# Optimization experiments

Measured on AMD Instinct MI355X. Metric: run time of the kernel, lower is better.

The kernel has to match this reference:

```python
import jax, jax.numpy as jnp
import numpy as np

N_NODES = 20000
N_EDGES = 320000
IN_DIM = 128
HID = 256
HEADS = 8
DH = HID // HEADS  # 32
LAYERS = 3
NUM_GRAPHS = 64
OUT_DIM = 10
SLOPE = 0.2  # DGL GATv2Conv default negative_slope


def setup_inputs() -> dict:
    key = jax.random.key(0)
    ks = jax.random.split(key, 20)
    s_in = 1.0 / np.sqrt(IN_DIM)
    s_h = 1.0 / np.sqrt(HID)
    s_h2 = 1.0 / np.sqrt(HID // 2)
    return {
        "feature": jax.random.normal(ks[0], (N_NODES, IN_DIM), jnp.float32),
        "W_in": jax.random.normal(ks[1], (IN_DIM, HID), jnp.float32) * s_in,
        "b_in": jax.random.normal(ks[2], (HID,), jnp.float32) * 0.01,
        "W_src": jax.random.normal(ks[3], (LAYERS, HID, HID), jnp.float32) * s_h,
        "b_src": jax.random.normal(ks[4], (LAYERS, HID), jnp.float32) * 0.01,
        "W_dst": jax.random.normal(ks[5], (LAYERS, HID, HID), jnp.float32) * s_h,
        "b_dst": jax.random.normal(ks[6], (LAYERS, HID), jnp.float32) * 0.01,
        "attn": jax.random.normal(ks[7], (LAYERS, HEADS, DH), jnp.float32) * (1.0 / np.sqrt(DH)),
        "Wc1": jax.random.normal(ks[8], (HID, HID), jnp.float32) * s_h,
        "bc1": jax.random.normal(ks[9], (HID,), jnp.float32) * 0.01,
        "Wc2": jax.random.normal(ks[10], (HID, HID // 2), jnp.float32) * s_h,
        "bc2": jax.random.normal(ks[11], (HID // 2,), jnp.float32) * 0.01,
        "Wc3": jax.random.normal(ks[12], (HID // 2, OUT_DIM), jnp.float32) * s_h2,
        "bc3": jax.random.normal(ks[13], (OUT_DIM,), jnp.float32) * 0.01,
        "src": jax.random.randint(ks[14], (N_EDGES,), 0, N_NODES, jnp.int32),
        "dst": jax.random.randint(ks[15], (N_EDGES,), 0, N_NODES, jnp.int32),
        "graph_ids": jnp.sort(jax.random.randint(ks[16], (N_NODES,), 0, NUM_GRAPHS, jnp.int32)),
    }


def _gatv2_layer(h, Ws, bs, Wd, bd, a, src, dst):
    # DGL GATv2Conv: e_ij = a^T LeakyReLU(W_src h_j + W_dst h_i), edge softmax over
    # incoming edges of dst, scatter-sum of alpha * W_src h_src; residual = Identity
    # (in_feats == heads*out_feats); activation relu.
    n = h.shape[0]
    fs = (h @ Ws + bs).reshape(n, HEADS, DH)  # [N,H,D]
    fd = (h @ Wd + bd).reshape(n, HEADS, DH)
    e = jax.nn.leaky_relu(fs[src] + fd[dst], SLOPE)          # [E,H,D]
    score = jnp.einsum("ehd,hd->eh", e, a)                   # [E,H]
    m = jax.ops.segment_max(score, dst, num_segments=n)       # stable softmax max
    ex = jnp.exp(score - m[dst])
    denom = jax.ops.segment_sum(ex, dst, num_segments=n)
    alpha = ex / denom[dst]                                    # [E,H]
    rst = jax.ops.segment_sum(alpha[:, :, None] * fs[src], dst, num_segments=n)
    out = jax.nn.relu(rst + h.reshape(n, HEADS, DH))          # residual + activation
    return out.reshape(n, HID)


def reference(feature, W_in, b_in, W_src, b_src, W_dst, b_dst, attn,
              Wc1, bc1, Wc2, bc2, Wc3, bc3, src, dst, graph_ids):
    h = feature @ W_in + b_in
    for l in range(LAYERS):
        h = _gatv2_layer(h, W_src[l], b_src[l], W_dst[l], b_dst[l], attn[l], src, dst)
    # dgl.sum_nodes over batched graph -> per-graph segment sum
    hg = jax.ops.segment_sum(h, graph_ids, num_segments=NUM_GRAPHS)  # [G,HID]
    # classifier (dropout is identity in eval mode)
    x = jax.nn.relu(hg @ Wc1 + bc1)
    x = jax.nn.relu(x @ Wc2 + bc2)
    return x @ Wc3 + bc3  # [G,OUT_DIM]
```

## Files before the change

### kernel.cpp

```cpp
#include <hip/hip_runtime.h>
#include <hip/hip_bf16.h>
#include <math.h>

#define N_NODES 20000
#define N_EDGES 320000
#define IN_DIM 128
#define HID 256
#define HEADS 8
#define DH 32
#define LAYERS 3
#define NUM_GRAPHS 64
#define OUT_DIM 10
#define SLOPE 0.2f

#define NBKT 5
#define N_BINS (N_NODES * NBKT)
#define N_BINS4 (N_BINS / 4)

#define CHUNK_I4 255
#define N_CHUNKS 99

#define GEMM_TILES 626
#define COUNT_BLOCKS 1250

typedef __bf16 bf16x8 __attribute__((ext_vector_type(8)));
typedef float f32x4 __attribute__((ext_vector_type(4)));

static __device__ __forceinline__ unsigned short f2bfbits(float v) {
    __bf16 b = (__bf16)v;
    return __builtin_bit_cast(unsigned short, b);
}
static __device__ __forceinline__ void unpack8(uint4 u, float* f) {
    unsigned p0 = u.x, p1 = u.y, p2 = u.z, p3 = u.w;
    f[0] = __builtin_bit_cast(float, p0 << 16);
    f[1] = __builtin_bit_cast(float, p0 & 0xffff0000u);
    f[2] = __builtin_bit_cast(float, p1 << 16);
    f[3] = __builtin_bit_cast(float, p1 & 0xffff0000u);
    f[4] = __builtin_bit_cast(float, p2 << 16);
    f[5] = __builtin_bit_cast(float, p2 & 0xffff0000u);
    f[6] = __builtin_bit_cast(float, p3 << 16);
    f[7] = __builtin_bit_cast(float, p3 & 0xffff0000u);
}

typedef const __attribute__((address_space(1))) unsigned int* as1_u32p;
typedef __attribute__((address_space(3))) unsigned int* as3_u32p;
static __device__ __forceinline__ void async_cp16(const unsigned short* g, unsigned short* l) {
    __builtin_amdgcn_global_load_lds((as1_u32p)g, (as3_u32p)l, 16, 0, 0);
}

#define CAST_N4 (N_NODES * IN_DIM / 4)
#define WTRANS_TOTAL (IN_DIM * HID + 6 * HID * HID)
#define PREP_TOTAL (CAST_N4 + WTRANS_TOTAL)
#define PREP_BLOCKS (PREP_TOTAL / 256)

static __device__ void prep_item(int idx,
                                 const float* __restrict__ feat,
                                 const float* __restrict__ Win,
                                 const float* __restrict__ Wsrc,
                                 const float* __restrict__ Wdst,
                                 unsigned short* __restrict__ featH,
                                 unsigned short* __restrict__ WinT,
                                 unsigned short* __restrict__ WT) {
    if (idx < CAST_N4) {
        float4 v = ((const float4*)feat)[idx];
        ushort4 o;
        o.x = f2bfbits(v.x); o.y = f2bfbits(v.y);
        o.z = f2bfbits(v.z); o.w = f2bfbits(v.w);
        ((ushort4*)featH)[idx] = o;
    } else {
        int j = idx - CAST_N4;
        if (j < IN_DIM * HID) {
            int n = j / IN_DIM, k = j % IN_DIM;
            WinT[j] = f2bfbits(Win[k * HID + n]);
        } else {
            int r6 = j - IN_DIM * HID;
            int mat = r6 >> 16;
            int r = r6 & 65535;
            int n = r >> 8, k = r & 255;
            const float* base = (mat < 3) ? (Wsrc + (size_t)mat * 65536)
                                          : (Wdst + (size_t)(mat - 3) * 65536);
            WT[r6] = f2bfbits(base[k * 256 + n]);
        }
    }
}

static __device__ void scans_unit(int u, int t, const int* __restrict__ cnt,
                                  int* __restrict__ cglob, int* __restrict__ offs,
                                  int* si) {
    int idx4 = u * CHUNK_I4 + t;
    bool act = (t < CHUNK_I4) && (idx4 < N_BINS4);
    int4 x = make_int4(0, 0, 0, 0);
    if (act) x = ((const int4*)cnt)[idx4];
    int tsum = x.x + x.y + x.z + x.w;
    int v = tsum;
#pragma unroll
    for (int d = 1; d < 64; d <<= 1) {
        int w = __shfl_up(v, d, 64);
        if ((t & 63) >= d) v += w;
    }
    if ((t & 63) == 63) si[4 + (t >> 6)] = v;
    __syncthreads();
    if (t == 0) {
        int S = si[4] + si[5] + si[6] + si[7];
        si[0] = atomicAdd(cglob, S);
    }
    __syncthreads();
    int base = si[0];
    int wid = t >> 6;
    int waveoff = 0;
    if (wid > 0) waveoff += si[4];
    if (wid > 1) waveoff += si[5];
    if (wid > 2) waveoff += si[6];
    int ex = base + waveoff + (v - tsum);
    if (act) {
        int4 o;
        o.x = ex; o.y = ex + x.x; o.z = o.y + x.y; o.w = o.z + x.z;
        ((int4*)offs)[idx4] = o;
    }
}

template <int DUAL>
static __device__ void gemm_tile(int mt, int nt, int t,
                                 const unsigned short* __restrict__ Ah,
                                 const unsigned short* __restrict__ BT1,
                                 const float* __restrict__ bias1,
                                 unsigned short* __restrict__ O1,
                                 const unsigned short* __restrict__ BT2,
                                 const float* __restrict__ bias2,
                                 unsigned short* __restrict__ O2,
                                 int M, int K, int N,
                                 unsigned short* Bs1P, unsigned short* Bs2P) {
    const int wv = t >> 6, lane = t & 63, quad = lane >> 4, l15 = lane & 15;
    const int m0 = mt * 64, n0 = nt * 128;

    const int sB0 = wv * 64 + lane, sB1v = sB0 + 256;
    const int rB0 = sB0 >> 2, cB0 = (sB0 & 3) ^ ((rB0 >> 1) & 3);
    const int rB1 = sB1v >> 2, cB1 = (sB1v & 3) ^ ((rB1 >> 1) & 3);
    const size_t offB0 = (size_t)(n0 + rB0) * K + cB0 * 8;
    const size_t offB1 = (size_t)(n0 + rB1) * K + cB1 * 8;

    auto issueB = [&](int buf, int k0) {
        async_cp16(BT1 + offB0 + k0, Bs1P + buf * 4096 + wv * 512);
        async_cp16(BT1 + offB1 + k0, Bs1P + buf * 4096 + 2048 + wv * 512);
        if (DUAL) {
            async_cp16(BT2 + offB0 + k0, Bs2P + buf * 4096 + wv * 512);
            async_cp16(BT2 + offB1 + k0, Bs2P + buf * 4096 + 2048 + wv * 512);
        }
    };

    const int mrow0 = (wv >> 1) * 32;
    const int ncb = (wv & 1) * 64;

    int r0 = m0 + mrow0 + l15;      if (r0 >= M) r0 = M - 1;
    int r1 = m0 + mrow0 + 16 + l15; if (r1 >= M) r1 = M - 1;
    const unsigned short* Ap0 = Ah + (size_t)r0 * K + quad * 8;
    const unsigned short* Ap1 = Ah + (size_t)r1 * K + quad * 8;

    f32x4 zero = {0.f, 0.f, 0.f, 0.f};
    f32x4 acc1[2][4], acc2[2][4];
#pragma unroll
    for (int mi = 0; mi < 2; ++mi)
#pragma unroll
        for (int t4 = 0; t4 < 4; ++t4) { acc1[mi][t4] = zero; acc2[mi][t4] = zero; }

    issueB(0, 0);
    bf16x8 aC0 = __builtin_bit_cast(bf16x8, *(const uint4*)(Ap0));
    bf16x8 aC1 = __builtin_bit_cast(bf16x8, *(const uint4*)(Ap1));

    int buf = 0;
    for (int k0 = 0; k0 < K; k0 += 32, buf ^= 1) {
        __syncthreads();
        bf16x8 aN0 = aC0, aN1 = aC1;
        if (k0 + 32 < K) {
            issueB(buf ^ 1, k0 + 32);
            aN0 = __builtin_bit_cast(bf16x8, *(const uint4*)(Ap0 + k0 + 32));
            aN1 = __builtin_bit_cast(bf16x8, *(const uint4*)(Ap1 + k0 + 32));
        }
#pragma unroll
        for (int t4 = 0; t4 < 4; ++t4) {
            int brow = ncb + t4 * 16 + l15;
            int boff = brow * 32 + ((quad ^ ((brow >> 1) & 3)) << 3);
            bf16x8 b1 = __builtin_bit_cast(bf16x8, *(const uint4*)(Bs1P + buf * 4096 + boff));
            acc1[0][t4] = __builtin_amdgcn_mfma_f32_16x16x32_bf16(aC0, b1, acc1[0][t4], 0, 0, 0);
            acc1[1][t4] = __builtin_amdgcn_mfma_f32_16x16x32_bf16(aC1, b1, acc1[1][t4], 0, 0, 0);
            if (DUAL) {
                bf16x8 b2 = __builtin_bit_cast(bf16x8, *(const uint4*)(Bs2P + buf * 4096 + boff));
                acc2[0][t4] = __builtin_amdgcn_mfma_f32_16x16x32_bf16(aC0, b2, acc2[0][t4], 0, 0, 0);
                acc2[1][t4] = __builtin_amdgcn_mfma_f32_16x16x32_bf16(aC1, b2, acc2[1][t4], 0, 0, 0);
            }
        }
        aC0 = aN0; aC1 = aN1;
    }

    float bia1[4], bia2[4];
#pragma unroll
    for (int t4 = 0; t4 < 4; ++t4) {
        bia1[t4] = bias1[n0 + ncb + t4 * 16 + l15];
        bia2[t4] = DUAL ? bias2[n0 + ncb + t4 * 16 + l15] : 0.f;
    }
#pragma unroll
    for (int mi = 0; mi < 2; ++mi) {
#pragma unroll
        for (int t4 = 0; t4 < 4; ++t4) {
            int gn = n0 + ncb + t4 * 16 + l15;
#pragma unroll
            for (int r = 0; r < 4; ++r) {
                int gm = m0 + mrow0 + mi * 16 + quad * 4 + r;
                if (gm < M) {
                    float v = acc1[mi][t4][r] + bia1[t4];
                    O1[(size_t)gm * N + gn] = f2bfbits(v);
                    if (DUAL) {
                        float v2 = acc2[mi][t4][r] + bia2[t4];
                        O2[(size_t)gm * N + gn] = f2bfbits(v2);
                    }
                }
            }
        }
    }
}

static __device__ void agg_unit(int u, int t,
                                const unsigned short* __restrict__ fsb,
                                const unsigned short* __restrict__ fdb,
                                unsigned short* __restrict__ hb,
                                const int* __restrict__ offs,
                                const int* __restrict__ cnt,
                                const int* __restrict__ csr_src,
                                const float* __restrict__ attn_l) {
    int node = u * 8 + (t >> 5);
    if (node >= N_NODES) return;
    int l32 = t & 31;
    int dbase = l32 * 8;
    int abase = (l32 >> 2) * DH + (l32 & 3) * 8;

    float a[8];
#pragma unroll
    for (int j = 0; j < 8; ++j) a[j] = attn_l[abase + j];

    float fdv[8];
    unpack8(*(const uint4*)(fdb + (size_t)node * HID + dbase), fdv);

    float ssum0 = 0.f, ssum1 = 0.f;
    float acc0[8], acc1[8];
#pragma unroll
    for (int j = 0; j < 8; ++j) { acc0[j] = 0.f; acc1[j] = 0.f; }

    auto procE = [&](uint4 uu, float* acc, float& ssum) {
        float fsv[8];
        unpack8(uu, fsv);
        float p = 0.f;
#pragma unroll
        for (int j = 0; j < 8; ++j) {
            float e = fsv[j] + fdv[j];
            e = fmaxf(e, SLOPE * e);
            p += e * a[j];
        }
        p += __shfl_xor(p, 1, 64);
        p += __shfl_xor(p, 2, 64);
        float w = __expf(p);
        ssum += w;
#pragma unroll
        for (int j = 0; j < 8; ++j) acc[j] += w * fsv[j];
    };

    const unsigned short* fsl = fsb + dbase;
    int b0 = node * NBKT;
    int beg = offs[b0];
    int end = offs[b0 + NBKT - 1] + cnt[b0 + NBKT - 1];
    int nfull = (end - beg) >> 2;
    const int limit = beg + nfull * 4;

    uint4 cu0, cu1, cu2, cu3;
    int ci0, ci1, ci2, ci3;
    int base = beg + 8;
    bool have = (nfull >= 1);
    bool haveN = (nfull >= 2);
    if (have) {
        int s0 = csr_src[beg], s1 = csr_src[beg + 1];
        int s2 = csr_src[beg + 2], s3 = csr_src[beg + 3];
        if (haveN) {
            ci0 = csr_src[beg + 4]; ci1 = csr_src[beg + 5];
            ci2 = csr_src[beg + 6]; ci3 = csr_src[beg + 7];
        }
        cu0 = *(const uint4*)(fsl + (size_t)s0 * HID);
        cu1 = *(const uint4*)(fsl + (size_t)s1 * HID);
        cu2 = *(const uint4*)(fsl + (size_t)s2 * HID);
        cu3 = *(const uint4*)(fsl + (size_t)s3 * HID);
    }
    while (have) {
        uint4 nu0, nu1, nu2, nu3;
        int ni0, ni1, ni2, ni3;
        if (haveN) {
            nu0 = *(const uint4*)(fsl + (size_t)ci0 * HID);
            nu1 = *(const uint4*)(fsl + (size_t)ci1 * HID);
            nu2 = *(const uint4*)(fsl + (size_t)ci2 * HID);
            nu3 = *(const uint4*)(fsl + (size_t)ci3 * HID);
        }
        bool haveNN = (base + 4 <= limit);
        if (haveNN) {
            ni0 = csr_src[base]; ni1 = csr_src[base + 1];
            ni2 = csr_src[base + 2]; ni3 = csr_src[base + 3];
        }
        base += 4;
        procE(cu0, acc0, ssum0);
        procE(cu1, acc1, ssum1);
        procE(cu2, acc0, ssum0);
        procE(cu3, acc1, ssum1);
        if (haveN) { cu0 = nu0; cu1 = nu1; cu2 = nu2; cu3 = nu3; }
        if (haveNN) { ci0 = ni0; ci1 = ni1; ci2 = ni2; ci3 = ni3; }
        have = haveN; haveN = haveNN;
    }
    for (int idx = limit; idx < end; ++idx) {
        int sv = csr_src[idx];
        procE(*(const uint4*)(fsl + (size_t)sv * HID), acc0, ssum0);
    }

    float ssum = ssum0 + ssum1;
    float acc[8];
#pragma unroll
    for (int j = 0; j < 8; ++j) acc[j] = acc0[j] + acc1[j];

    float inv = ssum > 0.f ? 1.f / ssum : 0.f;
    float hv[8];
    unpack8(*(const uint4*)(hb + (size_t)node * HID + dbase), hv);
    unsigned short ob[8];
#pragma unroll
    for (int j = 0; j < 8; ++j) {
        float o = fmaxf(acc[j] * inv + hv[j], 0.f);
        ob[j] = f2bfbits(o);
    }
    *(uint4*)(hb + (size_t)node * HID + dbase) = *(uint4*)ob;
}

__global__ void prep_count_kernel(const float* __restrict__ feat,
                                  const float* __restrict__ Win,
                                  const float* __restrict__ Wsrc,
                                  const float* __restrict__ Wdst,
                                  unsigned short* __restrict__ featH,
                                  unsigned short* __restrict__ WinT,
                                  unsigned short* __restrict__ WT,
                                  const int* __restrict__ src,
                                  const int* __restrict__ dst,
                                  int* __restrict__ cnt,
                                  int* __restrict__ slot) {
    int bid = blockIdx.x;
    if (bid < PREP_BLOCKS) {
        prep_item(bid * 256 + threadIdx.x, feat, Win, Wsrc, Wdst, featH, WinT, WT);
    } else {
        int e = (bid - PREP_BLOCKS) * 256 + threadIdx.x;
        if (e < N_EDGES) {
            int bin = dst[e] * NBKT + (src[e] >> 12);
            slot[e] = atomicAdd(&cnt[bin], 1);
        }
    }
}

__global__ __launch_bounds__(256, 4) void gemm0_scan_kernel(
    const unsigned short* __restrict__ featH, const unsigned short* __restrict__ WinT,
    const float* __restrict__ b_in, unsigned short* __restrict__ hb,
    const int* __restrict__ cnt, int* __restrict__ cglob,
    int* __restrict__ offs) {
    __shared__ __align__(16) unsigned short smem[8192];
    int bid = blockIdx.x;
    if (bid < GEMM_TILES) {
        gemm_tile<0>(bid >> 1, bid & 1, threadIdx.x, featH, WinT, b_in, hb,
                     (const unsigned short*)nullptr, (const float*)nullptr,
                     (unsigned short*)nullptr, N_NODES, IN_DIM, HID,
                     smem, smem);
    } else {
        scans_unit(bid - GEMM_TILES, threadIdx.x, cnt, cglob, offs,
                   (int*)(void*)smem);
    }
}

__global__ __launch_bounds__(256, 4) void gemm1_fill_kernel(
    const unsigned short* __restrict__ hb,
    const unsigned short* __restrict__ WTs, const float* __restrict__ bs,
    unsigned short* __restrict__ fsb,
    const unsigned short* __restrict__ WTd, const float* __restrict__ bd,
    unsigned short* __restrict__ fdb,
    const int* __restrict__ src, const int* __restrict__ dst,
    const int* __restrict__ offs, const int* __restrict__ slot,
    int* __restrict__ csr_src) {
    __shared__ __align__(16) unsigned short smem[16384];
    int bid = blockIdx.x;
    if (bid < GEMM_TILES) {
        gemm_tile<1>(bid >> 1, bid & 1, threadIdx.x, hb, WTs, bs, fsb, WTd, bd, fdb,
                     N_NODES, HID, HID, smem, smem + 8192);
    } else {
        int e = (bid - GEMM_TILES) * 256 + threadIdx.x;
        if (e < N_EDGES) {
            int sv = src[e];
            int bin = dst[e] * NBKT + (sv >> 12);
            csr_src[offs[bin] + slot[e]] = sv;
        }
    }
}

__global__ __launch_bounds__(256, 4) void gemm_kernel(
    const unsigned short* __restrict__ Ah,
    const unsigned short* __restrict__ BT1, const float* __restrict__ bias1,
    unsigned short* __restrict__ O1,
    const unsigned short* __restrict__ BT2, const float* __restrict__ bias2,
    unsigned short* __restrict__ O2) {
    __shared__ __align__(16) unsigned short smem[16384];
    gemm_tile<1>(blockIdx.x, blockIdx.y, threadIdx.x, Ah, BT1, bias1, O1,
                 BT2, bias2, O2, N_NODES, HID, HID, smem, smem + 8192);
}

__global__ __launch_bounds__(256) void agg_kernel(const unsigned short* __restrict__ fsb,
                                                  const unsigned short* __restrict__ fdb,
                                                  unsigned short* __restrict__ hb,
                                                  const int* __restrict__ offs,
                                                  const int* __restrict__ cnt,
                                                  const int* __restrict__ csr_src,
                                                  const float* __restrict__ attn_l) {
    int nwg = gridDim.x;
    int q = nwg >> 3, r = nwg & 7;
    int xcd = blockIdx.x & 7, idx = blockIdx.x >> 3;
    int u = (xcd < r) ? xcd * (q + 1) + idx
                      : r * (q + 1) + (xcd - r) * q + idx;
    agg_unit(u, threadIdx.x, fsb, fdb, hb, offs, cnt, csr_src, attn_l);
}

__global__ __launch_bounds__(256) void poolcls_kernel(
    const unsigned short* __restrict__ hb, const int* __restrict__ gid,
    const float* __restrict__ Wc1, const float* __restrict__ bc1,
    const float* __restrict__ Wc2, const float* __restrict__ bc2,
    const float* __restrict__ Wc3, const float* __restrict__ bc3,
    float* __restrict__ out) {
    __shared__ float part[8 * HID];
    __shared__ float xin[HID];
    __shared__ float x1[HID];
    __shared__ float x2[HID / 2];
    int g = blockIdx.x, t = threadIdx.x;

    int lo = 0, hi = N_NODES;
    while (lo < hi) { int mid = (lo + hi) >> 1; if (gid[mid] < g) lo = mid + 1; else hi = mid; }
    int s0 = lo;
    hi = N_NODES;
    while (lo < hi) { int mid = (lo + hi) >> 1; if (gid[mid] < g + 1) lo = mid + 1; else hi = mid; }
    int e0 = lo;

    int r = t >> 5;
    int fb = (t & 31) * 8;
    float a0[8], a1[8];
#pragma unroll
    for (int j = 0; j < 8; ++j) { a0[j] = 0.f; a1[j] = 0.f; }
    int n = s0 + r;
    for (; n + 8 < e0; n += 16) {
        uint4 u0 = *(const uint4*)(hb + (size_t)n * HID + fb);
        uint4 u1 = *(const uint4*)(hb + (size_t)(n + 8) * HID + fb);
        float f0[8], f1[8];
        unpack8(u0, f0); unpack8(u1, f1);
#pragma unroll
        for (int j = 0; j < 8; ++j) { a0[j] += f0[j]; a1[j] += f1[j]; }
    }
    if (n < e0) {
        uint4 u0 = *(const uint4*)(hb + (size_t)n * HID + fb);
        float f0[8];
        unpack8(u0, f0);
#pragma unroll
        for (int j = 0; j < 8; ++j) a0[j] += f0[j];
    }
#pragma unroll
    for (int j = 0; j < 8; ++j) part[r * HID + fb + j] = a0[j] + a1[j];
    __syncthreads();
    {
        float s = 0.f;
#pragma unroll
        for (int r2 = 0; r2 < 8; ++r2) s += part[r2 * HID + t];
        xin[t] = s;
    }
    __syncthreads();

    {
        float acc = bc1[t];
        for (int k = 0; k < HID; ++k) acc += xin[k] * Wc1[k * HID + t];
        x1[t] = fmaxf(acc, 0.f);
    }
    __syncthreads();
    if (t < HID / 2) {
        float acc = bc2[t];
        for (int k = 0; k < HID; ++k) acc += x1[k] * Wc2[k * (HID / 2) + t];
        x2[t] = fmaxf(acc, 0.f);
    }
    __syncthreads();
    if (t < OUT_DIM) {
        float acc = bc3[t];
        for (int k = 0; k < HID / 2; ++k) acc += x2[k] * Wc3[k * OUT_DIM + t];
        out[g * OUT_DIM + t] = acc;
    }
}

extern "C" void kernel_launch(void* const* d_in, const int* in_sizes, int n_in,
                              void* d_out, int out_size, void* d_ws, size_t ws_size,
                              hipStream_t stream) {
    const float* feature = (const float*)d_in[0];
    const float* W_in   = (const float*)d_in[1];
    const float* b_in   = (const float*)d_in[2];
    const float* W_src  = (const float*)d_in[3];
    const float* b_src  = (const float*)d_in[4];
    const float* W_dst  = (const float*)d_in[5];
    const float* b_dst  = (const float*)d_in[6];
    const float* attn   = (const float*)d_in[7];
    const float* Wc1    = (const float*)d_in[8];
    const float* bc1    = (const float*)d_in[9];
    const float* Wc2    = (const float*)d_in[10];
    const float* bc2    = (const float*)d_in[11];
    const float* Wc3    = (const float*)d_in[12];
    const float* bc3    = (const float*)d_in[13];
    const int* src     = (const int*)d_in[14];
    const int* dst     = (const int*)d_in[15];
    const int* gid     = (const int*)d_in[16];
    float* out = (float*)d_out;

    char* w = (char*)d_ws;
    auto alloc = [&](size_t bytes) -> void* {
        void* p = (void*)w;
        w += (bytes + 255) & ~(size_t)255;
        return p;
    };
    unsigned short* hb  = (unsigned short*)alloc((size_t)N_NODES * HID * 2);
    unsigned short* fsb = (unsigned short*)alloc((size_t)N_NODES * HID * 2);
    unsigned short* fdb = (unsigned short*)alloc((size_t)N_NODES * HID * 2);
    int* cnt     = (int*)alloc((size_t)N_BINS * 4);
    int* cglob   = (int*)alloc(4);
    int* offs    = (int*)alloc((size_t)(N_BINS + 4) * 4);
    int* slot    = (int*)alloc((size_t)N_EDGES * 4);
    int* csr_src = (int*)alloc((size_t)N_EDGES * 4);
    unsigned short* WinT = (unsigned short*)alloc((size_t)IN_DIM * HID * 2);
    unsigned short* WT   = (unsigned short*)alloc((size_t)6 * HID * HID * 2);
    unsigned short* featH = (unsigned short*)alloc((size_t)N_NODES * IN_DIM * 2);
    (void)alloc(4096);

    size_t zlen = (size_t)((char*)offs - (char*)cnt);
    hipMemsetAsync(cnt, 0, zlen, stream);

    hipLaunchKernelGGL(prep_count_kernel, dim3(PREP_BLOCKS + COUNT_BLOCKS), dim3(256), 0, stream,
                       feature, W_in, W_src, W_dst, featH, WinT, WT, src, dst, cnt, slot);

    hipLaunchKernelGGL(gemm0_scan_kernel, dim3(GEMM_TILES + N_CHUNKS), dim3(256), 0, stream,
                       featH, WinT, b_in, hb, cnt, cglob, offs);

    hipLaunchKernelGGL(gemm1_fill_kernel, dim3(GEMM_TILES + COUNT_BLOCKS), dim3(256), 0, stream,
                       hb, WT, b_src, fsb, WT + 3 * 65536, b_dst, fdb,
                       src, dst, offs, slot, csr_src);

    for (int l = 0; l < LAYERS; ++l) {
        hipLaunchKernelGGL(agg_kernel, dim3(N_NODES / 8), dim3(256), 0, stream,
                           fsb, fdb, hb, offs, cnt, csr_src, attn + (size_t)l * HEADS * DH);
        if (l + 1 < LAYERS) {
            hipLaunchKernelGGL(gemm_kernel, dim3(313, 2), dim3(256), 0, stream,
                               hb, WT + (size_t)(l + 1) * 65536, b_src + (size_t)(l + 1) * HID, fsb,
                               WT + (size_t)(4 + l) * 65536, b_dst + (size_t)(l + 1) * HID, fdb);
        }
    }

    hipLaunchKernelGGL(poolcls_kernel, dim3(NUM_GRAPHS), dim3(256), 0, stream,
                       hb, gid, Wc1, bc1, Wc2, bc2, Wc3, bc3, out);
}
```

Measured before the change: 312.3 us.

## Fuse graph sum-pooling into last aggregation; tile weight transpose through LDS

The last GATv2 aggregation layer now pools node outputs into per-graph sums directly. Each block reduces its 8 nodes by graph id in shared memory and adds the result to a global fp32 buffer with atomics, so the final bf16 h write/read and the separate pooling pass are gone and the classifier kernel only reads the pooled vector. The weight transpose and bf16 cast in the prep kernel is rewritten as a 64x32 tile transpose through padded LDS, giving coalesced reads and 16-byte writes. The trade-off is extra atomic traffic and a __syncthreads in the last aggregation kernel. The early-return for out-of-range nodes is removed, which is safe only because N_NODES divides evenly by 8.

```diff
diff --git a/kernel.cpp b/kernel.cpp
--- a/kernel.cpp
+++ b/kernel.cpp
@@ -23,6 +23,10 @@
 #define GEMM_TILES 626
 #define COUNT_BLOCKS 1250
 
+#define CAST_BLOCKS 2500
+#define WT_TILES (16 + 192)
+#define PREP_BLOCKS (CAST_BLOCKS + WT_TILES)
+
 typedef __bf16 bf16x8 __attribute__((ext_vector_type(8)));
 typedef float f32x4 __attribute__((ext_vector_type(4)));
 
@@ -46,42 +50,6 @@
 typedef __attribute__((address_space(3))) unsigned int* as3_u32p;
 static __device__ __forceinline__ void async_cp16(const unsigned short* g, unsigned short* l) {
     __builtin_amdgcn_global_load_lds((as1_u32p)g, (as3_u32p)l, 16, 0, 0);
-}
-
-#define CAST_N4 (N_NODES * IN_DIM / 4)
-#define WTRANS_TOTAL (IN_DIM * HID + 6 * HID * HID)
-#define PREP_TOTAL (CAST_N4 + WTRANS_TOTAL)
-#define PREP_BLOCKS (PREP_TOTAL / 256)
-
-static __device__ void prep_item(int idx,
-                                 const float* __restrict__ feat,
-                                 const float* __restrict__ Win,
-                                 const float* __restrict__ Wsrc,
-                                 const float* __restrict__ Wdst,
-                                 unsigned short* __restrict__ featH,
-                                 unsigned short* __restrict__ WinT,
-                                 unsigned short* __restrict__ WT) {
-    if (idx < CAST_N4) {
-        float4 v = ((const float4*)feat)[idx];
-        ushort4 o;
-        o.x = f2bfbits(v.x); o.y = f2bfbits(v.y);
-        o.z = f2bfbits(v.z); o.w = f2bfbits(v.w);
-        ((ushort4*)featH)[idx] = o;
-    } else {
-        int j = idx - CAST_N4;
-        if (j < IN_DIM * HID) {
-            int n = j / IN_DIM, k = j % IN_DIM;
-            WinT[j] = f2bfbits(Win[k * HID + n]);
-        } else {
-            int r6 = j - IN_DIM * HID;
-            int mat = r6 >> 16;
-            int r = r6 & 65535;
-            int n = r >> 8, k = r & 255;
-            const float* base = (mat < 3) ? (Wsrc + (size_t)mat * 65536)
-                                          : (Wdst + (size_t)(mat - 3) * 65536);
-            WT[r6] = f2bfbits(base[k * 256 + n]);
-        }
-    }
 }
 
 static __device__ void scans_unit(int u, int t, const int* __restrict__ cnt,
@@ -219,6 +187,7 @@
     }
 }
 
+template <int WRITEH>
 static __device__ void agg_unit(int u, int t,
                                 const unsigned short* __restrict__ fsb,
                                 const unsigned short* __restrict__ fdb,
@@ -226,9 +195,11 @@
                                 const int* __restrict__ offs,
                                 const int* __restrict__ cnt,
                                 const int* __restrict__ csr_src,
-                                const float* __restrict__ attn_l) {
+                                const float* __restrict__ attn_l,
+                                const int* __restrict__ gid,
+                                float* __restrict__ hg,
+                                float* part, int* gids) {
     int node = u * 8 + (t >> 5);
-    if (node >= N_NODES) return;
     int l32 = t & 31;
     int dbase = l32 * 8;
     int abase = (l32 >> 2) * DH + (l32 & 3) * 8;
@@ -323,31 +294,93 @@
     float inv = ssum > 0.f ? 1.f / ssum : 0.f;
     float hv[8];
     unpack8(*(const uint4*)(hb + (size_t)node * HID + dbase), hv);
-    unsigned short ob[8];
-#pragma unroll
-    for (int j = 0; j < 8; ++j) {
-        float o = fmaxf(acc[j] * inv + hv[j], 0.f);
-        ob[j] = f2bfbits(o);
-    }
-    *(uint4*)(hb + (size_t)node * HID + dbase) = *(uint4*)ob;
-}
-
-__global__ void prep_count_kernel(const float* __restrict__ feat,
-                                  const float* __restrict__ Win,
-                                  const float* __restrict__ Wsrc,
-                                  const float* __restrict__ Wdst,
-                                  unsigned short* __restrict__ featH,
-                                  unsigned short* __restrict__ WinT,
-                                  unsigned short* __restrict__ WT,
-                                  const int* __restrict__ src,
-                                  const int* __restrict__ dst,
-                                  int* __restrict__ cnt,
-                                  int* __restrict__ slot) {
+
+    if (WRITEH) {
+        unsigned short ob[8];
+#pragma unroll
+        for (int j = 0; j < 8; ++j) {
+            float o = fmaxf(acc[j] * inv + hv[j], 0.f);
+            ob[j] = f2bfbits(o);
+        }
+        *(uint4*)(hb + (size_t)node * HID + dbase) = *(uint4*)ob;
+    } else {
+        int w = t >> 5;
+#pragma unroll
+        for (int j = 0; j < 8; ++j)
+            part[w * HID + dbase + j] = fmaxf(acc[j] * inv + hv[j], 0.f);
+        if (l32 == 0) gids[w] = gid[node];
+        __syncthreads();
+        float run = 0.f;
+        int cur = gids[0];
+#pragma unroll
+        for (int w2 = 0; w2 < 8; ++w2) {
+            int g2 = gids[w2];
+            if (g2 != cur) {
+                atomicAdd(&hg[(size_t)cur * HID + t], run);
+                run = 0.f; cur = g2;
+            }
+            run += part[w2 * HID + t];
+        }
+        atomicAdd(&hg[(size_t)cur * HID + t], run);
+    }
+}
+
+__global__ __launch_bounds__(256) void prep_count_kernel(
+    const float* __restrict__ feat,
+    const float* __restrict__ Win,
+    const float* __restrict__ Wsrc,
+    const float* __restrict__ Wdst,
+    unsigned short* __restrict__ featH,
+    unsigned short* __restrict__ WinT,
+    unsigned short* __restrict__ WT,
+    const int* __restrict__ src,
+    const int* __restrict__ dst,
+    int* __restrict__ cnt,
+    int* __restrict__ slot) {
+    __shared__ float Lf[64 * 33];
     int bid = blockIdx.x;
-    if (bid < PREP_BLOCKS) {
-        prep_item(bid * 256 + threadIdx.x, feat, Win, Wsrc, Wdst, featH, WinT, WT);
+    int t = threadIdx.x;
+    if (bid < CAST_BLOCKS) {
+        int idx = bid * 256 + t;
+        float4 v = ((const float4*)feat)[idx];
+        ushort4 o;
+        o.x = f2bfbits(v.x); o.y = f2bfbits(v.y);
+        o.z = f2bfbits(v.z); o.w = f2bfbits(v.w);
+        ((ushort4*)featH)[idx] = o;
+    } else if (bid < PREP_BLOCKS) {
+        int b2 = bid - CAST_BLOCKS;
+        const float* S;
+        unsigned short* D;
+        int k0, n0, Kd;
+        if (b2 < 16) {
+            S = Win; D = WinT; Kd = IN_DIM;
+            k0 = (b2 >> 3) * 64; n0 = (b2 & 7) * 32;
+        } else {
+            b2 -= 16;
+            int mat = b2 >> 5, tt = b2 & 31;
+            S = (mat < 3) ? (Wsrc + (size_t)mat * 65536) : (Wdst + (size_t)(mat - 3) * 65536);
+            D = WT + (size_t)mat * 65536; Kd = HID;
+            k0 = (tt >> 3) * 64; n0 = (tt & 7) * 32;
+        }
+        {
+            int r = t >> 2, c = (t & 3) * 8;
+            const float* sp = S + (size_t)(k0 + r) * HID + n0 + c;
+            float4 v0 = *(const float4*)(sp);
+            float4 v1 = *(const float4*)(sp + 4);
+            float* lp = Lf + r * 33 + c;
+            lp[0] = v0.x; lp[1] = v0.y; lp[2] = v0.z; lp[3] = v0.w;
+            lp[4] = v1.x; lp[5] = v1.y; lp[6] = v1.z; lp[7] = v1.w;
+        }
+        __syncthreads();
+        {
+            int nn = t >> 3, kk = (t & 7) * 8;
+            unsigned short ob[8];
+#pragma unroll
+            for (int j = 0; j < 8; ++j) ob[j] = f2bfbits(Lf[(kk + j) * 33 + nn]);
+            *(uint4*)(D + (size_t)(n0 + nn) * Kd + k0 + kk) = *(uint4*)ob;
+        }
     } else {
-        int e = (bid - PREP_BLOCKS) * 256 + threadIdx.x;
+        int e = (bid - PREP_BLOCKS) * 256 + t;
         if (e < N_EDGES) {
             int bin = dst[e] * NBKT + (src[e] >> 12);
             slot[e] = atomicAdd(&cnt[bin], 1);
@@ -408,6 +441,13 @@
                  BT2, bias2, O2, N_NODES, HID, HID, smem, smem + 8192);
 }
 
+static __device__ __forceinline__ int xcd_swz(int b, int nwg) {
+    int q = nwg >> 3, r = nwg & 7;
+    int xcd = b & 7, idx = b >> 3;
+    return (xcd < r) ? xcd * (q + 1) + idx
+                     : r * (q + 1) + (xcd - r) * q + idx;
+}
+
 __global__ __launch_bounds__(256) void agg_kernel(const unsigned short* __restrict__ fsb,
                                                   const unsigned short* __restrict__ fdb,
                                                   unsigned short* __restrict__ hb,
@@ -415,65 +455,39 @@
                                                   const int* __restrict__ cnt,
                                                   const int* __restrict__ csr_src,
                                                   const float* __restrict__ attn_l) {
-    int nwg = gridDim.x;
-    int q = nwg >> 3, r = nwg & 7;
-    int xcd = blockIdx.x & 7, idx = blockIdx.x >> 3;
-    int u = (xcd < r) ? xcd * (q + 1) + idx
-                      : r * (q + 1) + (xcd - r) * q + idx;
-    agg_unit(u, threadIdx.x, fsb, fdb, hb, offs, cnt, csr_src, attn_l);
-}
-
-__global__ __launch_bounds__(256) void poolcls_kernel(
-    const unsigned short* __restrict__ hb, const int* __restrict__ gid,
+    int u = xcd_swz(blockIdx.x, gridDim.x);
+    agg_unit<1>(u, threadIdx.x, fsb, fdb, hb, offs, cnt, csr_src, attn_l,
+                nullptr, nullptr, nullptr, nullptr);
+}
+
+__global__ __launch_bounds__(256) void agg_pool_kernel(const unsigned short* __restrict__ fsb,
+                                                       const unsigned short* __restrict__ fdb,
+                                                       unsigned short* __restrict__ hb,
+                                                       const int* __restrict__ offs,
+                                                       const int* __restrict__ cnt,
+                                                       const int* __restrict__ csr_src,
+                                                       const float* __restrict__ attn_l,
+                                                       const int* __restrict__ gid,
+                                                       float* __restrict__ hg) {
+    __shared__ float part[8 * HID];
+    __shared__ int gids[8];
+    int u = xcd_swz(blockIdx.x, gridDim.x);
+    agg_unit<0>(u, threadIdx.x, fsb, fdb, hb, offs, cnt, csr_src, attn_l,
+                gid, hg, part, gids);
+}
+
+__global__ __launch_bounds__(256) void cls_kernel(
+    const float* __restrict__ hg,
     const float* __restrict__ Wc1, const float* __restrict__ bc1,
     const float* __restrict__ Wc2, const float* __restrict__ bc2,
     const float* __restrict__ Wc3, const float* __restrict__ bc3,
     float* __restrict__ out) {
-    __shared__ float part[8 * HID];
     __shared__ float xin[HID];
     __shared__ float x1[HID];
     __shared__ float x2[HID / 2];
     int g = blockIdx.x, t = threadIdx.x;
-
-    int lo = 0, hi = N_NODES;
-    while (lo < hi) { int mid = (lo + hi) >> 1; if (gid[mid] < g) lo = mid + 1; else hi = mid; }
-    int s0 = lo;
-    hi = N_NODES;
-    while (lo < hi) { int mid = (lo + hi) >> 1; if (gid[mid] < g + 1) lo = mid + 1; else hi = mid; }
-    int e0 = lo;
-
-    int r = t >> 5;
-    int fb = (t & 31) * 8;
-    float a0[8], a1[8];
-#pragma unroll
-    for (int j = 0; j < 8; ++j) { a0[j] = 0.f; a1[j] = 0.f; }
-    int n = s0 + r;
-    for (; n + 8 < e0; n += 16) {
-        uint4 u0 = *(const uint4*)(hb + (size_t)n * HID + fb);
-        uint4 u1 = *(const uint4*)(hb + (size_t)(n + 8) * HID + fb);
-        float f0[8], f1[8];
-        unpack8(u0, f0); unpack8(u1, f1);
-#pragma unroll
-        for (int j = 0; j < 8; ++j) { a0[j] += f0[j]; a1[j] += f1[j]; }
-    }
-    if (n < e0) {
-        uint4 u0 = *(const uint4*)(hb + (size_t)n * HID + fb);
-        float f0[8];
-        unpack8(u0, f0);
-#pragma unroll
-        for (int j = 0; j < 8; ++j) a0[j] += f0[j];
-    }
-#pragma unroll
-    for (int j = 0; j < 8; ++j) part[r * HID + fb + j] = a0[j] + a1[j];
+    xin[t] = hg[(size_t)g * HID + t];
     __syncthreads();
-    {
-        float s = 0.f;
-#pragma unroll
-        for (int r2 = 0; r2 < 8; ++r2) s += part[r2 * HID + t];
-        xin[t] = s;
-    }
-    __syncthreads();
-
     {
         float acc = bc1[t];
         for (int k = 0; k < HID; ++k) acc += xin[k] * Wc1[k * HID + t];
@@ -526,6 +540,7 @@
     unsigned short* fdb = (unsigned short*)alloc((size_t)N_NODES * HID * 2);
     int* cnt     = (int*)alloc((size_t)N_BINS * 4);
     int* cglob   = (int*)alloc(4);
+    float* hg    = (float*)alloc((size_t)NUM_GRAPHS * HID * 4);
     int* offs    = (int*)alloc((size_t)(N_BINS + 4) * 4);
     int* slot    = (int*)alloc((size_t)N_EDGES * 4);
     int* csr_src = (int*)alloc((size_t)N_EDGES * 4);
@@ -548,15 +563,19 @@
                        src, dst, offs, slot, csr_src);
 
     for (int l = 0; l < LAYERS; ++l) {
-        hipLaunchKernelGGL(agg_kernel, dim3(N_NODES / 8), dim3(256), 0, stream,
-                           fsb, fdb, hb, offs, cnt, csr_src, attn + (size_t)l * HEADS * DH);
         if (l + 1 < LAYERS) {
+            hipLaunchKernelGGL(agg_kernel, dim3(N_NODES / 8), dim3(256), 0, stream,
+                               fsb, fdb, hb, offs, cnt, csr_src, attn + (size_t)l * HEADS * DH);
             hipLaunchKernelGGL(gemm_kernel, dim3(313, 2), dim3(256), 0, stream,
                                hb, WT + (size_t)(l + 1) * 65536, b_src + (size_t)(l + 1) * HID, fsb,
                                WT + (size_t)(4 + l) * 65536, b_dst + (size_t)(l + 1) * HID, fdb);
-        }
-    }
-
-    hipLaunchKernelGGL(poolcls_kernel, dim3(NUM_GRAPHS), dim3(256), 0, stream,
-                       hb, gid, Wc1, bc1, Wc2, bc2, Wc3, bc3, out);
-}
+        } else {
+            hipLaunchKernelGGL(agg_pool_kernel, dim3(N_NODES / 8), dim3(256), 0, stream,
+                               fsb, fdb, hb, offs, cnt, csr_src, attn + (size_t)l * HEADS * DH,
+                               gid, hg);
+        }
+    }
+
+    hipLaunchKernelGGL(cls_kernel, dim3(NUM_GRAPHS), dim3(256), 0, stream,
+                       hg, Wc1, bc1, Wc2, bc2, Wc3, bc3, out);
+}
```

Result: faster. 304.1 us (-2.6%).
